# Kernel tuning notes

Measured on AMD Instinct MI355X. Metric: run time of the kernel, lower is better.

Reference implementation:

```python
import jax, jax.numpy as jnp
import numpy as np

NUM_CLASSES = 97  # vocab size; SOS token id == NUM_CLASSES
D = 512   # in_planes (xDim)
S = 512   # sDim (GRU hidden)
A = 512   # attDim == emdDim
T = 25    # max_len_labels == encoder length L
B = 2048  # batch


def setup_inputs() -> dict:
    key = jax.random.key(0)
    ks = jax.random.split(key, 15)
    r = lambda k, shp: jax.random.normal(k, shp, jnp.float32) * 0.05
    return dict(
        x=jax.random.normal(ks[0], (B, T, D), jnp.float32),
        targets=jax.random.randint(ks[1], (2, B, T), 0, NUM_CLASSES),  # (fwd, reversed)
        Wx=r(ks[2], (2, D, A)), bx=r(ks[3], (2, A)),
        Ws=r(ks[4], (2, S, A)), bs=r(ks[5], (2, A)),
        wv=r(ks[6], (2, A)), wvb=r(ks[7], (2,)),
        emb=r(ks[8], (2, NUM_CLASSES + 1, A)),
        Wih=r(ks[9], (2, 3 * S, D + A)), bih=r(ks[10], (2, 3 * S)),
        Whh=r(ks[11], (2, 3 * S, S)), bhh=r(ks[12], (2, 3 * S)),
        Wfc=r(ks[13], (2, NUM_CLASSES, S)), bfc=r(ks[14], (2, NUM_CLASSES)),
    )


def _decode(x, targets, Wx, bx, Ws, bs, wv, wvb, emb, Wih, bih, Whh, bhh, Wfc, bfc):
    """One DecoderUnit unrolled over T steps (teacher forcing). x: [B,L,D]."""
    Bn = x.shape[0]
    # xEmbed is step-invariant -> hoist out of the recurrence
    xProj = jnp.einsum('bld,da->bla', x, Wx) + bx  # [B,L,A]
    y0 = jnp.full((Bn, 1), NUM_CLASSES, dtype=targets.dtype)  # SOS at step 0
    y_seq = jnp.concatenate([y0, targets[:, :-1]], axis=1)     # [B,T]

    def step(s, y_prev):
        # Bahdanau attention
        sProj = s @ Ws + bs                                  # [B,A]
        e = jnp.tanh(sProj[:, None, :] + xProj) @ wv + wvb   # [B,L]
        alpha = jax.nn.softmax(e, axis=1)
        ctx = jnp.einsum('bl,bld->bd', alpha, x)             # [B,D]
        # single-step GRU (PyTorch gate convention: r, z, n)
        gin = jnp.concatenate([emb[y_prev], ctx], axis=1)    # [B, A+D]
        gi = gin @ Wih.T + bih                               # [B,3S]
        gh = s @ Whh.T + bhh
        ir, iz, inn = jnp.split(gi, 3, axis=1)
        hr, hz, hn = jnp.split(gh, 3, axis=1)
        r = jax.nn.sigmoid(ir + hr)
        z = jax.nn.sigmoid(iz + hz)
        n = jnp.tanh(inn + r * hn)
        s_new = (1.0 - z) * n + z * s
        return s_new, s_new @ Wfc.T + bfc                    # logits [B,C]

    s0 = jnp.zeros((Bn, S), x.dtype)
    _, outs = jax.lax.scan(step, s0, jnp.swapaxes(y_seq, 0, 1))  # [T,B,C]
    return jnp.swapaxes(outs, 0, 1)  # [B,T,C]


def reference(x, targets, Wx, bx, Ws, bs, wv, wvb, emb, Wih, bih, Whh, bhh, Wfc, bfc):
    # vmap over the 2 decoders (forward / reverse); x shared
    f = jax.vmap(_decode, in_axes=(None, 0) + (0,) * 13)
    return f(x, targets, Wx, bx, Ws, bs, wv, wvb, emb, Wih, bih, Whh, bhh, Wfc, bfc)  # [2,B,T,C]
```

## Files before the change

kernel.cpp:

```cpp
#include <hip/hip_runtime.h>
#include <hip/hip_fp16.h>

#define B_ 2048
#define T_ 25
#define CL_ 97

typedef float f32x4 __attribute__((ext_vector_type(4)));
typedef float f32x2 __attribute__((ext_vector_type(2)));
typedef _Float16 f16x8 __attribute__((ext_vector_type(8)));
typedef _Float16 f16x2 __attribute__((ext_vector_type(2)));

#define DI static __device__ __forceinline__

DI float fast_tanh(float x) { return 1.0f - 2.0f / (__expf(2.0f * x) + 1.0f); }
DI float fast_sigm(float x) { return 1.0f / (1.0f + __expf(-x)); }

DI void gl16(const void* g, void* l) {
    __builtin_amdgcn_global_load_lds((const __attribute__((address_space(1))) void*)g,
                                     (__attribute__((address_space(3))) void*)l, 16, 0, 0);
}


__global__ void k_convx(const float* __restrict__ x, _Float16* __restrict__ xh, int n8) {
    int i = blockIdx.x * 256 + threadIdx.x;
    if (i >= n8) return;
    const f32x4 v0 = *(const f32x4*)(x + (long long)i * 8);
    const f32x4 v1 = *(const f32x4*)(x + (long long)i * 8 + 4);
    f16x8 o;
    o[0] = (_Float16)v0[0]; o[1] = (_Float16)v0[1]; o[2] = (_Float16)v0[2]; o[3] = (_Float16)v0[3];
    o[4] = (_Float16)v1[0]; o[5] = (_Float16)v1[1]; o[6] = (_Float16)v1[2]; o[7] = (_Float16)v1[3];
    *(f16x8*)(xh + (long long)i * 8) = o;
}

__global__ void k_pack_w1(const float* __restrict__ Ws, const float* __restrict__ Whh,
                          const float* __restrict__ Wfc, const float* __restrict__ bs,
                          const float* __restrict__ bhh, const float* __restrict__ bfc,
                          _Float16* __restrict__ w1, float* __restrict__ b1) {
    int idx = blockIdx.x * 256 + threadIdx.x;
    if (idx >= 2 * 2176 * 64) return;
    const int k8 = idx & 63;
    const int n  = (idx >> 6) % 2176;
    const int g  = (idx >> 6) / 2176;
    const int k0 = k8 * 8;
    f16x8 o;
    if (n < 512) {
        const float* p = Ws + (long long)g * 512 * 512 + (long long)k0 * 512 + n;
        #pragma unroll
        for (int i = 0; i < 8; ++i) o[i] = (_Float16)p[(long long)i * 512];
    } else if (n < 2048) {
        const float* p = Whh + (long long)g * 1536 * 512 + (long long)(n - 512) * 512 + k0;
        #pragma unroll
        for (int i = 0; i < 8; ++i) o[i] = (_Float16)p[i];
    } else if (n < 2048 + CL_) {
        const float* p = Wfc + (long long)g * CL_ * 512 + (long long)(n - 2048) * 512 + k0;
        #pragma unroll
        for (int i = 0; i < 8; ++i) o[i] = (_Float16)p[i];
    } else {
        #pragma unroll
        for (int i = 0; i < 8; ++i) o[i] = (_Float16)0.0f;
    }
    *(f16x8*)(w1 + ((long long)g * 2176 + n) * 512 + k0) = o;
    if (k8 == 0) {
        float bv = (n < 512) ? bs[g * 512 + n]
                 : (n < 2048) ? bhh[g * 1536 + (n - 512)]
                 : (n < 2048 + CL_) ? bfc[g * CL_ + (n - 2048)] : 0.0f;
        b1[g * 2176 + n] = bv;
    }
}

__global__ void k_pack_w2(const float* __restrict__ Wih, _Float16* __restrict__ w2,
                          _Float16* __restrict__ w2e) {
    int idx = blockIdx.x * 256 + threadIdx.x;
    if (idx >= 2 * 1536 * 64) return;
    const int k8 = idx & 63;
    const int n  = (idx >> 6) % 1536;
    const int g  = (idx >> 6) / 1536;
    const int k0 = k8 * 8;
    const float* p = Wih + (long long)g * 1536 * 1024 + (long long)n * 1024;
    f16x8 o, oe;
    #pragma unroll
    for (int i = 0; i < 8; ++i) { o[i] = (_Float16)p[512 + k0 + i]; oe[i] = (_Float16)p[k0 + i]; }
    *(f16x8*)(w2  + ((long long)g * 1536 + n) * 512 + k0) = o;
    *(f16x8*)(w2e + ((long long)g * 1536 + n) * 512 + k0) = oe;
}

__global__ void k_pack_wx(const float* __restrict__ Wx, _Float16* __restrict__ wx) {
    int idx = blockIdx.x * 256 + threadIdx.x;
    if (idx >= 2 * 512 * 64) return;
    const int k8 = idx & 63;
    const int n  = (idx >> 6) & 511;
    const int g  = (idx >> 6) >> 9;
    const int k0 = k8 * 8;
    const float* p = Wx + (long long)g * 512 * 512 + (long long)k0 * 512 + n;
    f16x8 o;
    #pragma unroll
    for (int i = 0; i < 8; ++i) o[i] = (_Float16)p[(long long)i * 512];
    *(f16x8*)(wx + ((long long)g * 512 + n) * 512 + k0) = o;
}

__global__ void k_pack_emb(const float* __restrict__ emb, _Float16* __restrict__ embh) {
    int i = blockIdx.x * 256 + threadIdx.x;
    if (i >= 2 * 128 * 64) return;
    const int k8 = i & 63;
    const int y  = (i >> 6) & 127;
    const int g  = i >> 13;
    f16x8 o;
    if (y < 98) {
        const float* p = emb + (long long)(g * 98 + y) * 512 + k8 * 8;
        #pragma unroll
        for (int j = 0; j < 8; ++j) o[j] = (_Float16)p[j];
    } else {
        #pragma unroll
        for (int j = 0; j < 8; ++j) o[j] = (_Float16)0.0f;
    }
    *(f16x8*)(embh + (long long)(g * 128 + y) * 512 + k8 * 8) = o;
}

__global__ __launch_bounds__(256) void gemm_bt(
    const _Float16* __restrict__ A, long long aG,
    const _Float16* __restrict__ B, long long bG,
    float* __restrict__ Cf, _Float16* __restrict__ Ch,
    long long cG, int ldc,
    const float* __restrict__ bias, int biasG,
    int nblk_off, int n_split,
    float* __restrict__ lout, int lcols, int lldc)
{
    __shared__ _Float16 As[128 * 64];
    __shared__ _Float16 Bs[128 * 64];
    const int g  = blockIdx.z;
    const int m0 = blockIdx.y * 128;
    const int n0 = (blockIdx.x + nblk_off) * 128;
    const _Float16* Ag = A + (long long)g * aG + (long long)m0 * 512;
    const _Float16* Bg = B + (long long)g * bG + (long long)n0 * 512;
    const int tid  = threadIdx.x;
    const int lane = tid & 63, w = tid >> 6;
    const int wr = w >> 1, wc = w & 1;
    const int lr = lane & 15, kg = lane >> 4;
    const int srow = (lane >> 3);
    const int scol = (lane & 7) * 8;

    f32x4 acc[4][4];
    #pragma unroll
    for (int m = 0; m < 4; ++m)
        #pragma unroll
        for (int n = 0; n < 4; ++n) acc[m][n] = (f32x4)0.0f;

    for (int kt = 0; kt < 8; ++kt) {
        const int k0 = kt * 64;
        __syncthreads();
        #pragma unroll
        for (int cc = 0; cc < 4; ++cc) {
            const int r = w * 32 + cc * 8;
            gl16(Ag + (long long)(r + srow) * 512 + k0 + scol, &As[r * 64]);
            gl16(Bg + (long long)(r + srow) * 512 + k0 + scol, &Bs[r * 64]);
        }
        __syncthreads();
        #pragma unroll
        for (int kk = 0; kk < 2; ++kk) {
            f16x8 af[4], bf[4];
            #pragma unroll
            for (int m = 0; m < 4; ++m) af[m] = *(const f16x8*)&As[(wr * 64 + m * 16 + lr) * 64 + kk * 32 + kg * 8];
            #pragma unroll
            for (int n = 0; n < 4; ++n) bf[n] = *(const f16x8*)&Bs[(wc * 64 + n * 16 + lr) * 64 + kk * 32 + kg * 8];
            #pragma unroll
            for (int m = 0; m < 4; ++m)
                #pragma unroll
                for (int n = 0; n < 4; ++n)
                    acc[m][n] = __builtin_amdgcn_mfma_f32_16x16x32_f16(af[m], bf[n], acc[m][n], 0, 0, 0);
        }
    }

    #pragma unroll
    for (int n = 0; n < 4; ++n) {
        const int col = n0 + wc * 64 + n * 16 + lr;
        const float bb = bias ? bias[g * biasG + col] : 0.0f;
        if (col < n_split) {
            #pragma unroll
            for (int m = 0; m < 4; ++m) {
                const int row = m0 + wr * 64 + m * 16 + kg * 4;
                #pragma unroll
                for (int i = 0; i < 4; ++i) {
                    const long long off = (long long)g * cG + (long long)(row + i) * ldc + col;
                    const float v = acc[m][n][i] + bb;
                    if (Ch) Ch[off] = (_Float16)v; else Cf[off] = v;
                }
            }
        } else if (lout != nullptr) {
            const int c = col - n_split;
            if (c < lcols) {
                #pragma unroll
                for (int m = 0; m < 4; ++m) {
                    const int row = m0 + wr * 64 + m * 16 + kg * 4;
                    #pragma unroll
                    for (int i = 0; i < 4; ++i)
                        lout[(long long)(g * B_ + row + i) * lldc + c] = acc[m][n][i] + bb;
                }
            }
        }
    }
}

__global__ __launch_bounds__(256) void k_att(
    const _Float16* __restrict__ Yh,
    const _Float16* __restrict__ xpj,
    const _Float16* __restrict__ xh,
    const float* __restrict__ wv,
    _Float16* __restrict__ ctxh)
{
    const int b = blockIdx.x, g = blockIdx.z;
    const int tid = threadIdx.x, lane = tid & 63, w = tid >> 6;
    __shared__ float eL[25];
    const _Float16* sp = Yh + (long long)(g * B_ + b) * 2048;
    const float* wvg = wv + g * 512;
    const int a0 = lane * 8;
    const f16x8 spv = *(const f16x8*)(sp + a0);
    const f32x4 wv0 = *(const f32x4*)(wvg + a0);
    const f32x4 wv1 = *(const f32x4*)(wvg + a0 + 4);
    const _Float16* xpb = xpj + (long long)(g * B_ + b) * 25 * 512;
    for (int l = w; l < 25; l += 4) {
        const f16x8 xv = *(const f16x8*)(xpb + l * 512 + a0);
        float part = 0.0f;
        #pragma unroll
        for (int i = 0; i < 4; ++i) {
            part += fast_tanh((float)spv[i]     + (float)xv[i])     * wv0[i];
            part += fast_tanh((float)spv[4 + i] + (float)xv[4 + i]) * wv1[i];
        }
        #pragma unroll
        for (int off = 32; off > 0; off >>= 1) part += __shfl_xor(part, off);
        if (lane == 0) eL[l] = part;
    }
    __syncthreads();
    float m = -1e30f;
    #pragma unroll
    for (int l = 0; l < 25; ++l) m = fmaxf(m, eL[l]);
    float al[25], ssum = 0.0f;
    #pragma unroll
    for (int l = 0; l < 25; ++l) { al[l] = __expf(eL[l] - m); ssum += al[l]; }
    const float inv = 1.0f / ssum;
    const _Float16* xb = xh + (long long)b * 25 * 512;
    const int d0 = tid * 2;
    float c0 = 0.0f, c1 = 0.0f;
    #pragma unroll
    for (int l = 0; l < 25; ++l) {
        const f16x2 xv = *(const f16x2*)(xb + l * 512 + d0);
        c0 += al[l] * (float)xv[0];
        c1 += al[l] * (float)xv[1];
    }
    f16x2 o; o[0] = (_Float16)(c0 * inv); o[1] = (_Float16)(c1 * inv);
    *(f16x2*)(ctxh + (long long)(g * B_ + b) * 512 + d0) = o;
}

__global__ void k_gate(const _Float16* __restrict__ Yh,
                       const _Float16* __restrict__ Y2h,
                       const float* __restrict__ eW,
                       const int* __restrict__ tgt,
                       float* __restrict__ s32, _Float16* __restrict__ sh, int t)
{
    const int idx = blockIdx.x * 256 + threadIdx.x;
    if (idx >= 2 * B_ * 256) return;
    const int jp = (idx & 255) * 2;
    const int b  = (idx >> 8) & (B_ - 1);
    const int g  = idx >> 19;
    const int y  = (t == 0) ? CL_ : tgt[(g * B_ + b) * T_ + t - 1];
    const float*    ew = eW  + (long long)(g * 128 + y) * 1536;
    const _Float16* y2 = Y2h + (long long)(g * B_ + b) * 1536;
    const _Float16* yy = Yh  + (long long)(g * B_ + b) * 2048;
    const f32x2 ewr = *(const f32x2*)(ew + jp);
    const f32x2 ewz = *(const f32x2*)(ew + 512 + jp);
    const f32x2 ewn = *(const f32x2*)(ew + 1024 + jp);
    const f16x2 y2r = *(const f16x2*)(y2 + jp);
    const f16x2 y2z = *(const f16x2*)(y2 + 512 + jp);
    const f16x2 y2n = *(const f16x2*)(y2 + 1024 + jp);
    const f16x2 ghr = *(const f16x2*)(yy + 512 + jp);
    const f16x2 ghz = *(const f16x2*)(yy + 1024 + jp);
    const f16x2 ghn = *(const f16x2*)(yy + 1536 + jp);
    const long long si = (long long)(g * B_ + b) * 512 + jp;
    const f32x2 so = *(const f32x2*)(s32 + si);
    f32x2 sn;
    f16x2 snh;
    #pragma unroll
    for (int i = 0; i < 2; ++i) {
        const float r  = fast_sigm(ewr[i] + (float)y2r[i] + (float)ghr[i]);
        const float z  = fast_sigm(ewz[i] + (float)y2z[i] + (float)ghz[i]);
        const float nn = fast_tanh(ewn[i] + (float)y2n[i] + r * (float)ghn[i]);
        sn[i]  = (1.0f - z) * nn + z * so[i];
        snh[i] = (_Float16)sn[i];
    }
    *(f32x2*)(s32 + si) = sn;
    *(f16x2*)(sh + si) = snh;
}

extern "C" void kernel_launch(void* const* d_in, const int* in_sizes, int n_in,
                              void* d_out, int out_size, void* d_ws, size_t ws_size,
                              hipStream_t stream)
{
    (void)in_sizes; (void)n_in; (void)out_size;
    const float* x   = (const float*)d_in[0];
    const int*   tgt = (const int*)d_in[1];
    const float* Wx  = (const float*)d_in[2];
    const float* bx  = (const float*)d_in[3];
    const float* Wsm = (const float*)d_in[4];
    const float* bs  = (const float*)d_in[5];
    const float* wv  = (const float*)d_in[6];
    const float* emb = (const float*)d_in[8];
    const float* Wih = (const float*)d_in[9];
    const float* bih = (const float*)d_in[10];
    const float* Whh = (const float*)d_in[11];
    const float* bhh = (const float*)d_in[12];
    const float* Wfc = (const float*)d_in[13];
    const float* bfc = (const float*)d_in[14];
    float* out = (float*)d_out;

    char* base = (char*)d_ws;
    size_t off = 0;
    auto alloc = [&](size_t bytes) -> void* {
        void* r = base + off;
        off = (off + bytes + 255) & ~(size_t)255;
        return r;
    };
    _Float16* xh   = (_Float16*)alloc((size_t)B_ * T_ * 512 * 2);
    _Float16* xpj  = (_Float16*)alloc((size_t)2 * B_ * T_ * 512 * 2);
    _Float16* w1   = (_Float16*)alloc((size_t)2 * 2176 * 512 * 2);
    _Float16* w2   = (_Float16*)alloc((size_t)2 * 1536 * 512 * 2);
    _Float16* w2e  = (_Float16*)alloc((size_t)2 * 1536 * 512 * 2);
    _Float16* wx   = (_Float16*)alloc((size_t)2 * 512 * 512 * 2);
    _Float16* embh = (_Float16*)alloc((size_t)2 * 128 * 512 * 2);
    float*    b1   = (float*)alloc((size_t)2 * 2176 * 4);
    float*    eW   = (float*)alloc((size_t)2 * 128 * 1536 * 4);
    float*    s32  = (float*)alloc((size_t)2 * B_ * 512 * 4);
    _Float16* sh   = (_Float16*)alloc((size_t)2 * B_ * 512 * 2);
    _Float16* ctx  = (_Float16*)alloc((size_t)2 * B_ * 512 * 2);
    _Float16* Yh   = (_Float16*)alloc((size_t)2 * B_ * 2048 * 2);
    _Float16* Y2h  = (_Float16*)alloc((size_t)2 * B_ * 1536 * 2);
    if (off > ws_size) return;

    hipMemsetAsync(s32, 0, (size_t)2 * B_ * 512 * 4, stream);
    hipMemsetAsync(sh,  0, (size_t)2 * B_ * 512 * 2, stream);

    k_convx   <<<12800, 256, 0, stream>>>(x, xh, (B_ * T_ * 512) / 8);
    k_pack_w1 <<<1088, 256, 0, stream>>>(Wsm, Whh, Wfc, bs, bhh, bfc, w1, b1);
    k_pack_w2 <<<768, 256, 0, stream>>>(Wih, w2, w2e);
    k_pack_wx <<<256, 256, 0, stream>>>(Wx, wx);
    k_pack_emb<<<64, 256, 0, stream>>>(emb, embh);

    gemm_bt<<<dim3(12, 1, 2), 256, 0, stream>>>(
        embh, 128ll * 512, w2e, 1536ll * 512, eW, nullptr,
        128ll * 1536, 1536, bih, 1536, 0, 1 << 30, nullptr, 0, 0);

    gemm_bt<<<dim3(4, 400, 2), 256, 0, stream>>>(
        xh, 0ll, wx, 512ll * 512, nullptr, xpj, (long long)B_ * T_ * 512, 512,
        bx, 512, 0, 1 << 30, nullptr, 0, 0);

    for (int t = 0; t < T_; ++t) {
        gemm_bt<<<dim3(t > 0 ? 17 : 16, 16, 2), 256, 0, stream>>>(
            sh, (long long)B_ * 512, w1, 2176ll * 512, nullptr, Yh,
            (long long)B_ * 2048, 2048, b1, 2176, 0, 2048,
            t > 0 ? out + (long long)(t - 1) * CL_ : nullptr, CL_, T_ * CL_);
        k_att<<<dim3(B_, 1, 2), 256, 0, stream>>>(Yh, xpj, xh, wv, ctx);
        gemm_bt<<<dim3(12, 16, 2), 256, 0, stream>>>(
            ctx, (long long)B_ * 512, w2, 1536ll * 512, nullptr, Y2h,
            (long long)B_ * 1536, 1536, nullptr, 0, 0, 1 << 30, nullptr, 0, 0);
        k_gate<<<4096, 256, 0, stream>>>(Yh, Y2h, eW, tgt, s32, sh, t);
    }
    gemm_bt<<<dim3(1, 16, 2), 256, 0, stream>>>(
        sh, (long long)B_ * 512, w1, 2176ll * 512, nullptr, Yh,
        (long long)B_ * 2048, 2048, b1, 2176, 16, 2048,
        out + 24ll * CL_, CL_, T_ * CL_);
}
```

Baseline: 2.834 ms.

## Double-buffer and swizzle GEMM LDS tiles; fuse both decoders in attention kernel

```diff
diff --git a/kernel.cpp b/kernel.cpp
--- a/kernel.cpp
+++ b/kernel.cpp
@@ -125,8 +125,8 @@
     int nblk_off, int n_split,
     float* __restrict__ lout, int lcols, int lldc)
 {
-    __shared__ _Float16 As[128 * 64];
-    __shared__ _Float16 Bs[128 * 64];
+    __shared__ _Float16 As[2][128 * 64];
+    __shared__ _Float16 Bs[2][128 * 64];
     const int g  = blockIdx.z;
     const int m0 = blockIdx.y * 128;
     const int n0 = (blockIdx.x + nblk_off) * 128;
@@ -136,8 +136,8 @@
     const int lane = tid & 63, w = tid >> 6;
     const int wr = w >> 1, wc = w & 1;
     const int lr = lane & 15, kg = lane >> 4;
-    const int srow = (lane >> 3);
-    const int scol = (lane & 7) * 8;
+    const int srow = lane >> 3;
+    const int scol = (((lane & 7) ^ srow) * 8);
 
     f32x4 acc[4][4];
     #pragma unroll
@@ -145,29 +145,47 @@
         #pragma unroll
         for (int n = 0; n < 4; ++n) acc[m][n] = (f32x4)0.0f;
 
-    for (int kt = 0; kt < 8; ++kt) {
+    auto stage = [&](int buf, int kt) {
         const int k0 = kt * 64;
-        __syncthreads();
         #pragma unroll
         for (int cc = 0; cc < 4; ++cc) {
             const int r = w * 32 + cc * 8;
-            gl16(Ag + (long long)(r + srow) * 512 + k0 + scol, &As[r * 64]);
-            gl16(Bg + (long long)(r + srow) * 512 + k0 + scol, &Bs[r * 64]);
-        }
-        __syncthreads();
+            gl16(Ag + (long long)(r + srow) * 512 + k0 + scol, &As[buf][r * 64]);
+            gl16(Bg + (long long)(r + srow) * 512 + k0 + scol, &Bs[buf][r * 64]);
+        }
+    };
+
+    stage(0, 0);
+    #pragma unroll
+    for (int kt = 0; kt < 8; ++kt) {
+        const int cur = kt & 1;
+        if (kt < 7) {
+            stage(cur ^ 1, kt + 1);
+            asm volatile("s_waitcnt vmcnt(8)" ::: "memory");
+        } else {
+            asm volatile("s_waitcnt vmcnt(0)" ::: "memory");
+        }
+        __builtin_amdgcn_s_barrier();
         #pragma unroll
         for (int kk = 0; kk < 2; ++kk) {
             f16x8 af[4], bf[4];
             #pragma unroll
-            for (int m = 0; m < 4; ++m) af[m] = *(const f16x8*)&As[(wr * 64 + m * 16 + lr) * 64 + kk * 32 + kg * 8];
-            #pragma unroll
-            for (int n = 0; n < 4; ++n) bf[n] = *(const f16x8*)&Bs[(wc * 64 + n * 16 + lr) * 64 + kk * 32 + kg * 8];
+            for (int m = 0; m < 4; ++m) {
+                const int R = wr * 64 + m * 16 + lr;
+                af[m] = *(const f16x8*)&As[cur][R * 64 + (((kk * 4 + kg) ^ (R & 7)) * 8)];
+            }
+            #pragma unroll
+            for (int n = 0; n < 4; ++n) {
+                const int R = wc * 64 + n * 16 + lr;
+                bf[n] = *(const f16x8*)&Bs[cur][R * 64 + (((kk * 4 + kg) ^ (R & 7)) * 8)];
+            }
             #pragma unroll
             for (int m = 0; m < 4; ++m)
                 #pragma unroll
                 for (int n = 0; n < 4; ++n)
                     acc[m][n] = __builtin_amdgcn_mfma_f32_16x16x32_f16(af[m], bf[n], acc[m][n], 0, 0, 0);
         }
+        __builtin_amdgcn_s_barrier();
     }
 
     #pragma unroll
@@ -207,47 +225,87 @@
     const float* __restrict__ wv,
     _Float16* __restrict__ ctxh)
 {
-    const int b = blockIdx.x, g = blockIdx.z;
+    const int b = blockIdx.x;
     const int tid = threadIdx.x, lane = tid & 63, w = tid >> 6;
-    __shared__ float eL[25];
-    const _Float16* sp = Yh + (long long)(g * B_ + b) * 2048;
-    const float* wvg = wv + g * 512;
+    __shared__ float eL[2][28];
+    __shared__ float red[2][4][512];
     const int a0 = lane * 8;
-    const f16x8 spv = *(const f16x8*)(sp + a0);
-    const f32x4 wv0 = *(const f32x4*)(wvg + a0);
-    const f32x4 wv1 = *(const f32x4*)(wvg + a0 + 4);
-    const _Float16* xpb = xpj + (long long)(g * B_ + b) * 25 * 512;
-    for (int l = w; l < 25; l += 4) {
-        const f16x8 xv = *(const f16x8*)(xpb + l * 512 + a0);
-        float part = 0.0f;
-        #pragma unroll
-        for (int i = 0; i < 4; ++i) {
-            part += fast_tanh((float)spv[i]     + (float)xv[i])     * wv0[i];
-            part += fast_tanh((float)spv[4 + i] + (float)xv[4 + i]) * wv1[i];
-        }
-        #pragma unroll
-        for (int off = 32; off > 0; off >>= 1) part += __shfl_xor(part, off);
-        if (lane == 0) eL[l] = part;
+
+    #pragma unroll
+    for (int g = 0; g < 2; ++g) {
+        const _Float16* sp = Yh + (long long)(g * B_ + b) * 2048;
+        const f16x8 spv = *(const f16x8*)(sp + a0);
+        const float* wvg = wv + g * 512;
+        const f32x4 wv0 = *(const f32x4*)(wvg + a0);
+        const f32x4 wv1 = *(const f32x4*)(wvg + a0 + 4);
+        const _Float16* xpb = xpj + (long long)(g * B_ + b) * 25 * 512;
+        for (int l = w; l < 25; l += 4) {
+            const f16x8 xv = *(const f16x8*)(xpb + l * 512 + a0);
+            float part = 0.0f;
+            #pragma unroll
+            for (int i = 0; i < 4; ++i) {
+                part += fast_tanh((float)spv[i]     + (float)xv[i])     * wv0[i];
+                part += fast_tanh((float)spv[4 + i] + (float)xv[4 + i]) * wv1[i];
+            }
+            #pragma unroll
+            for (int off = 32; off > 0; off >>= 1) part += __shfl_xor(part, off);
+            if (lane == 0) eL[g][l] = part;
+        }
     }
     __syncthreads();
-    float m = -1e30f;
-    #pragma unroll
-    for (int l = 0; l < 25; ++l) m = fmaxf(m, eL[l]);
-    float al[25], ssum = 0.0f;
-    #pragma unroll
-    for (int l = 0; l < 25; ++l) { al[l] = __expf(eL[l] - m); ssum += al[l]; }
-    const float inv = 1.0f / ssum;
+
+    float al0[25], al1[25];
+    float m0 = -1e30f, m1 = -1e30f;
+    #pragma unroll
+    for (int l = 0; l < 25; ++l) { m0 = fmaxf(m0, eL[0][l]); m1 = fmaxf(m1, eL[1][l]); }
+    float ss0 = 0.0f, ss1 = 0.0f;
+    #pragma unroll
+    for (int l = 0; l < 25; ++l) {
+        al0[l] = __expf(eL[0][l] - m0); ss0 += al0[l];
+        al1[l] = __expf(eL[1][l] - m1); ss1 += al1[l];
+    }
+    const float inv0 = 1.0f / ss0, inv1 = 1.0f / ss1;
+
+    float c0[8], c1[8];
+    #pragma unroll
+    for (int j = 0; j < 8; ++j) { c0[j] = 0.0f; c1[j] = 0.0f; }
     const _Float16* xb = xh + (long long)b * 25 * 512;
-    const int d0 = tid * 2;
-    float c0 = 0.0f, c1 = 0.0f;
     #pragma unroll
     for (int l = 0; l < 25; ++l) {
-        const f16x2 xv = *(const f16x2*)(xb + l * 512 + d0);
-        c0 += al[l] * (float)xv[0];
-        c1 += al[l] * (float)xv[1];
-    }
-    f16x2 o; o[0] = (_Float16)(c0 * inv); o[1] = (_Float16)(c1 * inv);
-    *(f16x2*)(ctxh + (long long)(g * B_ + b) * 512 + d0) = o;
+        if ((l & 3) == w) {
+            const f16x8 xv = *(const f16x8*)(xb + l * 512 + a0);
+            #pragma unroll
+            for (int j = 0; j < 8; ++j) {
+                const float xf = (float)xv[j];
+                c0[j] += al0[l] * xf;
+                c1[j] += al1[l] * xf;
+            }
+        }
+    }
+    f32x4 p;
+    #pragma unroll
+    for (int h = 0; h < 2; ++h) {
+        #pragma unroll
+        for (int i = 0; i < 4; ++i) p[i] = c0[h * 4 + i] * inv0;
+        *(f32x4*)&red[0][w][a0 + h * 4] = p;
+        #pragma unroll
+        for (int i = 0; i < 4; ++i) p[i] = c1[h * 4 + i] * inv1;
+        *(f32x4*)&red[1][w][a0 + h * 4] = p;
+    }
+    __syncthreads();
+
+    const int c = tid * 2;
+    f32x2 s0 = {0.0f, 0.0f}, s1 = {0.0f, 0.0f};
+    #pragma unroll
+    for (int ww = 0; ww < 4; ++ww) {
+        s0 += *(const f32x2*)&red[0][ww][c];
+        s1 += *(const f32x2*)&red[1][ww][c];
+    }
+    f16x2 o0, o1;
+    o0[0] = (_Float16)s0[0]; o0[1] = (_Float16)s0[1];
+    o1[0] = (_Float16)s1[0]; o1[1] = (_Float16)s1[1];
+    *(f16x2*)(ctxh + (long long)b * 512 + c) = o0;
+    *(f16x2*)(ctxh + (long long)(B_ + b) * 512 + c) = o1;
 }
 
 __global__ void k_gate(const _Float16* __restrict__ Yh,
@@ -356,7 +414,7 @@
             sh, (long long)B_ * 512, w1, 2176ll * 512, nullptr, Yh,
             (long long)B_ * 2048, 2048, b1, 2176, 0, 2048,
             t > 0 ? out + (long long)(t - 1) * CL_ : nullptr, CL_, T_ * CL_);
-        k_att<<<dim3(B_, 1, 2), 256, 0, stream>>>(Yh, xpj, xh, wv, ctx);
+        k_att<<<dim3(B_, 1, 1), 256, 0, stream>>>(Yh, xpj, xh, wv, ctx);
         gemm_bt<<<dim3(12, 16, 2), 256, 0, stream>>>(
             ctx, (long long)B_ * 512, w2, 1536ll * 512, nullptr, Y2h,
             (long long)B_ * 1536, 1536, nullptr, 0, 0, 1 << 30, nullptr, 0, 0);
```

After: 2.987 ms. +5.4%, slower.
